# Kernel tuning notes

Measured on AMD Instinct MI355X. Metric: run time of the kernel, lower is better.

## Reference

```python
import jax, jax.numpy as jnp
import numpy as np

SCALE = 1.0 / 4.0      # alpha / dim
MULTIPLIER = 1.0

def _act(h):
    return jax.nn.gelu(h, approximate=False)  # torch nn.GELU(approximate='none')

def setup_inputs() -> dict:
    key = jax.random.key(0)
    ks = jax.random.split(key, 9)
    B, T, D = 64, 77, 768
    N, R = 1024, 4
    return {
        "x":     jax.random.normal(ks[0], (B, T, D), jnp.float32),
        "W_org": jax.random.normal(ks[1], (D, D), jnp.float32) * 0.02,
        "b_org": jax.random.normal(ks[2], (D,), jnp.float32) * 0.02,
        "w1":    jax.random.normal(ks[3], (N, D, R), jnp.float32) * 0.02,
        "b1":    jax.random.normal(ks[4], (N, R), jnp.float32) * 0.02,
        "mid_w": jax.random.normal(ks[5], (N, R, R), jnp.float32) * 0.02,
        "mid_b": jax.random.normal(ks[6], (N, R), jnp.float32) * 0.02,
        "w_out": jax.random.normal(ks[7], (N, R, D), jnp.float32) * 0.02,
        "b_out": jax.random.normal(ks[8], (N, D), jnp.float32) * 0.02,
    }

def reference(x, W_org, b_org, w1, b1, mid_w, mid_b, w_out, b_out):
    # per-concept low-rank MLP: h in [B, T, N, R]
    h = jnp.einsum('btd,ndh->btnh', x, w1) + b1[None, None]
    h = _act(h)
    # repeated 'h' in 'nhh' takes the diagonal of mid_w (elementwise scale),
    # exactly matching torch.einsum semantics in the source.
    h = jnp.einsum('btnh,nhh->btnh', h, mid_w) + mid_b[None, None]
    h = _act(h)
    # fuse out-projection with sum over concepts: sum_n (h_n @ w_out_n) + sum_n b_out_n
    up = jnp.einsum('btnh,nhd->btd', h, w_out) + jnp.sum(b_out, axis=0)
    org = x @ W_org.T + b_org
    return org + up * (MULTIPLIER * SCALE)
```

## Files before the change

kernel.cpp:

```cpp
#include <hip/hip_runtime.h>
#include <hip/hip_bf16.h>

#define M_TOK 4928
#define M_PAD 5120
#define M_GMM 4992
#define D_DIM 768
#define NR    4096

typedef __bf16 bf16;
typedef unsigned char u8;
typedef __attribute__((ext_vector_type(8))) __bf16 bf16x8;
typedef __attribute__((ext_vector_type(4))) float f32x4;
typedef __attribute__((address_space(1))) uint32_t gu32;
typedef __attribute__((address_space(3))) uint32_t su32;

#define GLDS(P, LDSP) \
  __builtin_amdgcn_global_load_lds((gu32*)(P), (su32*)(LDSP), 16, 0, 0)

__device__ __forceinline__ uint32_t pk_fp8x4(float a, float b, float c, float d) {
  uint32_t w = 0;
  w = (uint32_t)__builtin_amdgcn_cvt_pk_fp8_f32(a, b, (int)w, false);
  w = (uint32_t)__builtin_amdgcn_cvt_pk_fp8_f32(c, d, (int)w, true);
  return w;
}

__device__ __forceinline__ float act_fast(float v) {
  float e = __builtin_amdgcn_exp2f(v * -2.4554677f);
  return v * __builtin_amdgcn_rcpf(1.0f + e);
}

__device__ __forceinline__ int xcd_swizzle(int orig, int nwg) {
  const int q = nwg >> 3, r = nwg & 7;
  const int x = orig & 7, rest = orig >> 3;
  return (x < r ? x * (q + 1) : r * (q + 1) + (x - r) * q) + rest;
}


__global__ __launch_bounds__(256) void k_prep_x(const float* __restrict__ x,
                                                bf16* __restrict__ Xb) {
  int idx = (blockIdx.x * 256 + threadIdx.x) * 4;
  if (idx >= M_PAD * D_DIM) return;
  int m = idx / D_DIM;
  union { uint2 u; bf16 h[4]; } o;
  if (m < M_TOK) {
    float4 v = *(const float4*)(x + idx);
    o.h[0] = (bf16)v.x; o.h[1] = (bf16)v.y; o.h[2] = (bf16)v.z; o.h[3] = (bf16)v.w;
  } else {
    o.h[0] = o.h[1] = o.h[2] = o.h[3] = (bf16)0.0f;
  }
  *(uint2*)(Xb + idx) = o.u;
}

__global__ __launch_bounds__(256) void k_prep_xq(const float* __restrict__ x,
                                                 u8* __restrict__ Xq) {
  int idx = (blockIdx.x * 256 + threadIdx.x) * 4;
  if (idx >= M_PAD * D_DIM) return;
  int m = idx / D_DIM;
  uint32_t w = 0;
  if (m < M_TOK) {
    float4 v = *(const float4*)(x + idx);
    w = pk_fp8x4(v.x, v.y, v.z, v.w);
  }
  *(uint32_t*)(Xq + idx) = w;
}

__global__ __launch_bounds__(256) void k_prep_w1q(const float* __restrict__ w1,
                                                  u8* __restrict__ W1q) {
  int gid = blockIdx.x * 256 + threadIdx.x;
  int n = gid / 96, oct = gid % 96;
  const float4* src = (const float4*)w1 + (size_t)n * D_DIM + oct * 8;
  float e[4][8];
#pragma unroll
  for (int d = 0; d < 8; ++d) {
    float4 v = src[d];
    e[0][d] = v.x * 64.0f; e[1][d] = v.y * 64.0f;
    e[2][d] = v.z * 64.0f; e[3][d] = v.w * 64.0f;
  }
  size_t base = (size_t)n * 4 * D_DIM + oct * 8;
#pragma unroll
  for (int r = 0; r < 4; ++r) {
    uint2 o;
    o.x = pk_fp8x4(e[r][0], e[r][1], e[r][2], e[r][3]);
    o.y = pk_fp8x4(e[r][4], e[r][5], e[r][6], e[r][7]);
    *(uint2*)(W1q + base + (size_t)r * D_DIM) = o;
  }
}

__global__ __launch_bounds__(256) void k_prep_w2q(const float* __restrict__ w_out,
                                                  u8* __restrict__ W2q) {
  __shared__ float S[64 * 65];
  const int bk = blockIdx.x & 63, bd = blockIdx.x >> 6;
  const int k0 = bk * 64, d0 = bd * 64;
  const int tr = threadIdx.x >> 4;
  const int tc = (threadIdx.x & 15) * 4;
#pragma unroll
  for (int p = 0; p < 4; ++p) {
    const int kr = tr + p * 16;
    float4 v = *(const float4*)(w_out + (size_t)(k0 + kr) * D_DIM + d0 + tc);
    S[kr * 65 + tc + 0] = v.x; S[kr * 65 + tc + 1] = v.y;
    S[kr * 65 + tc + 2] = v.z; S[kr * 65 + tc + 3] = v.w;
  }
  __syncthreads();
#pragma unroll
  for (int p = 0; p < 4; ++p) {
    const int dr = tr + p * 16;
    uint32_t w = pk_fp8x4(16.0f * S[(tc + 0) * 65 + dr], 16.0f * S[(tc + 1) * 65 + dr],
                          16.0f * S[(tc + 2) * 65 + dr], 16.0f * S[(tc + 3) * 65 + dr]);
    *(uint32_t*)(W2q + (size_t)(d0 + dr) * NR + k0 + tc) = w;
  }
}

__global__ __launch_bounds__(256) void k_prep_worg(const float* __restrict__ W_org,
                                                   bf16* __restrict__ WorgB) {
  int idx = (blockIdx.x * 256 + threadIdx.x) * 4;
  if (idx >= D_DIM * D_DIM) return;
  float4 v = *(const float4*)(W_org + idx);
  union { uint2 u; bf16 h[4]; } o;
  o.h[0] = (bf16)v.x; o.h[1] = (bf16)v.y; o.h[2] = (bf16)v.z; o.h[3] = (bf16)v.w;
  *(uint2*)(WorgB + idx) = o.u;
}

__global__ __launch_bounds__(256) void k_bias_partial(const float* __restrict__ b_out,
                                                      float* __restrict__ partial) {
  int b = blockIdx.x;
  for (int d = threadIdx.x; d < D_DIM; d += 256) {
    float s = 0.0f;
    for (int n = b * 32; n < b * 32 + 32; ++n) s += b_out[n * D_DIM + d];
    partial[b * D_DIM + d] = s;
  }
}

__global__ __launch_bounds__(256) void k_bias_final2(const float* __restrict__ partial,
                                                     const float* __restrict__ b_org,
                                                     const float* __restrict__ mid_w,
                                                     float* __restrict__ bias_total,
                                                     float* __restrict__ diag) {
  int b = blockIdx.x;
  if (b < 3) {
    int d = b * 256 + threadIdx.x;
    if (d >= D_DIM) return;
    float s = 0.0f;
#pragma unroll
    for (int p = 0; p < 32; ++p) s += partial[p * D_DIM + d];
    bias_total[d] = b_org[d] + 0.25f * s;
  } else {
    int j = (b - 3) * 256 + threadIdx.x;
    diag[j] = mid_w[(j >> 2) * 16 + (j & 3) * 5];
  }
}


#define G1F_IT(S_, DO_STG, LAST_)                                               \
  {                                                                             \
    if (LAST_) { asm volatile("s_waitcnt vmcnt(0)" ::: "memory"); }             \
    else       { asm volatile("s_waitcnt vmcnt(4)" ::: "memory"); }             \
    asm volatile("s_barrier" ::: "memory");                                     \
    long a0[4], a1[4], b0[4], b1[4];                                            \
    _Pragma("unroll") for (int i = 0; i < 4; ++i) {                             \
      a0[i] = *(const long*)(&As[S_][aOff + i * 1024]);                         \
      a1[i] = *(const long*)(&As[S_][(aOff ^ 32) + i * 1024]);                  \
    }                                                                           \
    _Pragma("unroll") for (int j = 0; j < 4; ++j) {                             \
      b0[j] = *(const long*)(&Bs[S_][bOff + j * 1024]);                         \
      b1[j] = *(const long*)(&Bs[S_][(bOff ^ 32) + j * 1024]);                  \
    }                                                                           \
    if (DO_STG) {                                                               \
      GLDS(aP0, &As[((S_) + 2) % 3][ldsC0]);                                    \
      GLDS(aP1, &As[((S_) + 2) % 3][ldsC1]);                                    \
      GLDS(bP0, &Bs[((S_) + 2) % 3][ldsC0]);                                    \
      GLDS(bP1, &Bs[((S_) + 2) % 3][ldsC1]);                                    \
      aP0 += 64; aP1 += 64; bP0 += 64; bP1 += 64;                               \
    }                                                                           \
    _Pragma("unroll") for (int i = 0; i < 4; ++i)                               \
      _Pragma("unroll") for (int j = 0; j < 4; ++j)                             \
        acc[i][j] = __builtin_amdgcn_mfma_f32_16x16x32_fp8_fp8(b0[j], a0[i], acc[i][j], 0, 0, 0); \
    _Pragma("unroll") for (int i = 0; i < 4; ++i)                               \
      _Pragma("unroll") for (int j = 0; j < 4; ++j)                             \
        acc[i][j] = __builtin_amdgcn_mfma_f32_16x16x32_fp8_fp8(b1[j], a1[i], acc[i][j], 0, 0, 0); \
  }

__global__ __launch_bounds__(256) void k_gemm1(const u8* __restrict__ Xq,
                                               const u8* __restrict__ W1q,
                                               u8* __restrict__ H2q,
                                               const float* __restrict__ b1,
                                               const float* __restrict__ diag,
                                               const float* __restrict__ midb) {
  __shared__ u8 As[3][128 * 64];
  __shared__ u8 Bs[3][128 * 64];
  const int wgid = xcd_swizzle(blockIdx.x, 39 * 32);
  const int bmt = wgid >> 5;
  const int bnt = wgid & 31;
  const int m0 = bmt * 128, n0 = bnt * 128;
  const int lane = threadIdx.x & 63;
  const int wave = threadIdx.x >> 6;
  const int wm = wave >> 1, wn = wave & 1;
  const int lr = lane & 15, kg = lane >> 4;
  const int slotB = (((kg >> 1) ^ ((lr >> 1) & 3)) << 4) + ((kg & 1) << 3);
  const int aOff = (wm * 64 + lr) * 64 + slotB;
  const int bOff = (wn * 64 + lr) * 64 + slotB;

  const int src_slot = (lane & 3) ^ ((lane >> 3) & 3);
  const int srow = (wave * 2) * 16 + (lane >> 2);
  const u8* aP0 = Xq  + (size_t)(m0 + srow) * D_DIM + (src_slot << 4);
  const u8* aP1 = aP0 + 16 * D_DIM;
  const u8* bP0 = W1q + (size_t)(n0 + srow) * D_DIM + (src_slot << 4);
  const u8* bP1 = bP0 + 16 * D_DIM;
  const int ldsC0 = (wave * 2) * 1024, ldsC1 = ldsC0 + 1024;

  f32x4 acc[4][4];
#pragma unroll
  for (int i = 0; i < 4; ++i)
#pragma unroll
    for (int j = 0; j < 4; ++j) acc[i][j] = (f32x4)(0.0f);

  GLDS(aP0, &As[0][ldsC0]); GLDS(aP1, &As[0][ldsC1]);
  GLDS(bP0, &Bs[0][ldsC0]); GLDS(bP1, &Bs[0][ldsC1]);
  aP0 += 64; aP1 += 64; bP0 += 64; bP1 += 64;
  GLDS(aP0, &As[1][ldsC0]); GLDS(aP1, &As[1][ldsC1]);
  GLDS(bP0, &Bs[1][ldsC0]); GLDS(bP1, &Bs[1][ldsC1]);
  aP0 += 64; aP1 += 64; bP0 += 64; bP1 += 64;

  for (int g = 0; g < 3; ++g) {
    G1F_IT(0, true, false)
    G1F_IT(1, true, false)
    G1F_IT(2, true, false)
  }
  G1F_IT(0, true, false)
  G1F_IT(1, false, false)
  G1F_IT(2, false, true)

#pragma unroll
  for (int j = 0; j < 4; ++j) {
    const int jcb = n0 + wn * 64 + j * 16 + kg * 4;
    const float4 b1v = *(const float4*)(b1 + jcb);
    const float4 dgv = *(const float4*)(diag + jcb);
    const float4 mbv = *(const float4*)(midb + jcb);
#pragma unroll
    for (int i = 0; i < 4; ++i) {
      const int mr = m0 + wm * 64 + i * 16 + lr;
      float h, f0, f1, f2, f3;
      h = act_fast(fmaf(acc[i][j][0], 0.015625f, b1v.x)); f0 = act_fast(h * dgv.x + mbv.x);
      h = act_fast(fmaf(acc[i][j][1], 0.015625f, b1v.y)); f1 = act_fast(h * dgv.y + mbv.y);
      h = act_fast(fmaf(acc[i][j][2], 0.015625f, b1v.z)); f2 = act_fast(h * dgv.z + mbv.z);
      h = act_fast(fmaf(acc[i][j][3], 0.015625f, b1v.w)); f3 = act_fast(h * dgv.w + mbv.w);
      uint32_t w = pk_fp8x4(f0 * 128.0f, f1 * 128.0f, f2 * 128.0f, f3 * 128.0f);
      *(uint32_t*)(H2q + (size_t)mr * NR + jcb) = w;
    }
  }
}

__global__ __launch_bounds__(256) void k_gemm2a(const u8* __restrict__ H2q,
                                                const u8* __restrict__ W2q,
                                                bf16* __restrict__ padd) {
  __shared__ u8 As[3][128 * 64];
  __shared__ u8 Bs[3][128 * 64];
  const int wgid = xcd_swizzle(blockIdx.x, 39 * 6 * 4);
  const int bmt = wgid / 24;
  const int rem = wgid % 24;
  const int ks  = rem / 6;
  const int bnt = rem % 6;
  const int m0 = bmt * 128, n0 = bnt * 128;
  const int kbase = ks * 1024;
  const int lane = threadIdx.x & 63;
  const int wave = threadIdx.x >> 6;
  const int wm = wave >> 1, wn = wave & 1;
  const int lr = lane & 15, kg = lane >> 4;
  const int slotB = (((kg >> 1) ^ ((lr >> 1) & 3)) << 4) + ((kg & 1) << 3);
  const int aOff = (wm * 64 + lr) * 64 + slotB;
  const int bOff = (wn * 64 + lr) * 64 + slotB;

  const int src_slot = (lane & 3) ^ ((lane >> 3) & 3);
  const int srow = (wave * 2) * 16 + (lane >> 2);
  const u8* aP0 = H2q + (size_t)(m0 + srow) * NR + kbase + (src_slot << 4);
  const u8* aP1 = aP0 + 16 * NR;
  const u8* bP0 = W2q + (size_t)(n0 + srow) * NR + kbase + (src_slot << 4);
  const u8* bP1 = bP0 + 16 * NR;
  const int ldsC0 = (wave * 2) * 1024, ldsC1 = ldsC0 + 1024;

  f32x4 acc[4][4];
#pragma unroll
  for (int i = 0; i < 4; ++i)
#pragma unroll
    for (int j = 0; j < 4; ++j) acc[i][j] = (f32x4)(0.0f);

  GLDS(aP0, &As[0][ldsC0]); GLDS(aP1, &As[0][ldsC1]);
  GLDS(bP0, &Bs[0][ldsC0]); GLDS(bP1, &Bs[0][ldsC1]);
  aP0 += 64; aP1 += 64; bP0 += 64; bP1 += 64;
  GLDS(aP0, &As[1][ldsC0]); GLDS(aP1, &As[1][ldsC1]);
  GLDS(bP0, &Bs[1][ldsC0]); GLDS(bP1, &Bs[1][ldsC1]);
  aP0 += 64; aP1 += 64; bP0 += 64; bP1 += 64;

  for (int g = 0; g < 4; ++g) {
    G1F_IT(0, true, false)
    G1F_IT(1, true, false)
    G1F_IT(2, true, false)
  }
  G1F_IT(0, true, false)
  G1F_IT(1, true, false)
  G1F_IT(2, false, false)
  G1F_IT(0, false, true)

  bf16* dst = padd + (size_t)ks * M_TOK * D_DIM;
#pragma unroll
  for (int j = 0; j < 4; ++j) {
    const int cb = n0 + wn * 64 + j * 16 + kg * 4;
#pragma unroll
    for (int i = 0; i < 4; ++i) {
      const int mr = m0 + wm * 64 + i * 16 + lr;
      if (mr < M_TOK) {
        union { uint2 u; bf16 h[4]; } o;
        o.h[0] = (bf16)(acc[i][j][0] * 4.8828125e-4f);
        o.h[1] = (bf16)(acc[i][j][1] * 4.8828125e-4f);
        o.h[2] = (bf16)(acc[i][j][2] * 4.8828125e-4f);
        o.h[3] = (bf16)(acc[i][j][3] * 4.8828125e-4f);
        *(uint2*)(dst + (size_t)mr * D_DIM + cb) = o.u;
      }
    }
  }
}


#define G1B_IT(S_, DO_STG, LAST_)                                               \
  {                                                                             \
    if (LAST_) { asm volatile("s_waitcnt vmcnt(0)" ::: "memory"); }             \
    else       { asm volatile("s_waitcnt vmcnt(4)" ::: "memory"); }             \
    asm volatile("s_barrier" ::: "memory");                                     \
    bf16x8 a_[4], b_[4];                                                        \
    _Pragma("unroll") for (int i = 0; i < 4; ++i)                               \
      a_[i] = *(const bf16x8*)(&As[S_][aOff + i * 512]);                        \
    _Pragma("unroll") for (int j = 0; j < 4; ++j)                               \
      b_[j] = *(const bf16x8*)(&Bs[S_][bOff + j * 512]);                        \
    if (DO_STG) {                                                               \
      GLDS(aP0, &As[((S_) + 2) % 3][ldsC0]);                                    \
      GLDS(aP1, &As[((S_) + 2) % 3][ldsC1]);                                    \
      GLDS(bP0, &Bs[((S_) + 2) % 3][ldsC0]);                                    \
      GLDS(bP1, &Bs[((S_) + 2) % 3][ldsC1]);                                    \
      aP0 += 32; aP1 += 32; bP0 += 32; bP1 += 32;                               \
    }                                                                           \
    _Pragma("unroll") for (int i = 0; i < 4; ++i)                               \
      _Pragma("unroll") for (int j = 0; j < 4; ++j)                             \
        acc[i][j] = __builtin_amdgcn_mfma_f32_16x16x32_bf16(b_[j], a_[i], acc[i][j], 0, 0, 0); \
  }

__global__ __launch_bounds__(256) void k_gemm2b(const bf16* __restrict__ Xb,
                                                const bf16* __restrict__ WorgB,
                                                float* __restrict__ out,
                                                const float* __restrict__ bias) {
  __shared__ bf16 As[3][128 * 32];
  __shared__ bf16 Bs[3][128 * 32];
  const int wgid = xcd_swizzle(blockIdx.x, 39 * 6);
  const int bmt = wgid / 6;
  const int bnt = wgid % 6;
  const int m0 = bmt * 128, n0 = bnt * 128;
  const int lane = threadIdx.x & 63;
  const int wave = threadIdx.x >> 6;
  const int wm = wave >> 1, wn = wave & 1;
  const int lr = lane & 15, kg = lane >> 4;
  const int slot = (kg ^ ((lr >> 1) & 3)) << 3;
  const int aOff = (wm * 64 + lr) * 32 + slot;
  const int bOff = (wn * 64 + lr) * 32 + slot;

  const int src_slot = (lane & 3) ^ ((lane >> 3) & 3);
  const int srow = (wave * 2) * 16 + (lane >> 2);
  const bf16* aP0 = Xb    + (size_t)(m0 + srow) * D_DIM + (src_slot << 3);
  const bf16* aP1 = aP0 + 16 * D_DIM;
  const bf16* bP0 = WorgB + (size_t)(n0 + srow) * D_DIM + (src_slot << 3);
  const bf16* bP1 = bP0 + 16 * D_DIM;
  const int ldsC0 = (wave * 2) * 512, ldsC1 = ldsC0 + 512;

  f32x4 acc[4][4];
#pragma unroll
  for (int i = 0; i < 4; ++i)
#pragma unroll
    for (int j = 0; j < 4; ++j) acc[i][j] = (f32x4)(0.0f);

  GLDS(aP0, &As[0][ldsC0]); GLDS(aP1, &As[0][ldsC1]);
  GLDS(bP0, &Bs[0][ldsC0]); GLDS(bP1, &Bs[0][ldsC1]);
  aP0 += 32; aP1 += 32; bP0 += 32; bP1 += 32;
  GLDS(aP0, &As[1][ldsC0]); GLDS(aP1, &As[1][ldsC1]);
  GLDS(bP0, &Bs[1][ldsC0]); GLDS(bP1, &Bs[1][ldsC1]);
  aP0 += 32; aP1 += 32; bP0 += 32; bP1 += 32;

  for (int g = 0; g < 7; ++g) {
    G1B_IT(0, true, false)
    G1B_IT(1, true, false)
    G1B_IT(2, true, false)
  }
  G1B_IT(0, true, false)
  G1B_IT(1, false, false)
  G1B_IT(2, false, true)

#pragma unroll
  for (int j = 0; j < 4; ++j) {
    const int cb = n0 + wn * 64 + j * 16 + kg * 4;
    const f32x4 bv = *(const f32x4*)(bias + cb);
#pragma unroll
    for (int i = 0; i < 4; ++i) {
      const int mr = m0 + wm * 64 + i * 16 + lr;
      if (mr < M_TOK) {
        f32x4 o = acc[i][j] + bv;
        *(f32x4*)(out + (size_t)mr * D_DIM + cb) = o;
      }
    }
  }
}

__global__ __launch_bounds__(256) void k_reduce(const bf16* __restrict__ padd,
                                                float* __restrict__ out) {
  int idx = (blockIdx.x * 256 + threadIdx.x) * 4;
  if (idx >= M_TOK * D_DIM) return;
  float4 s = *(const float4*)(out + idx);
#pragma unroll
  for (int p = 0; p < 4; ++p) {
    union { uint2 u; bf16 h[4]; } v;
    v.u = *(const uint2*)(padd + (size_t)p * M_TOK * D_DIM + idx);
    s.x += (float)v.h[0]; s.y += (float)v.h[1];
    s.z += (float)v.h[2]; s.w += (float)v.h[3];
  }
  *(float4*)(out + idx) = s;
}


extern "C" void kernel_launch(void* const* d_in, const int* in_sizes, int n_in,
                              void* d_out, int out_size, void* d_ws, size_t ws_size,
                              hipStream_t stream) {
  const float* x     = (const float*)d_in[0];
  const float* W_org = (const float*)d_in[1];
  const float* b_org = (const float*)d_in[2];
  const float* w1    = (const float*)d_in[3];
  const float* b1    = (const float*)d_in[4];
  const float* mid_w = (const float*)d_in[5];
  const float* mid_b = (const float*)d_in[6];
  const float* w_out = (const float*)d_in[7];
  const float* b_out = (const float*)d_in[8];
  float* out = (float*)d_out;

  bf16* Xb    = (bf16*)d_ws;
  bf16* WorgB = Xb + (size_t)M_PAD * D_DIM;
  float* bias    = (float*)(WorgB + (size_t)D_DIM * D_DIM);
  float* partial = bias + 1024;
  float* diag    = partial + 32 * D_DIM;
  u8* Xq   = (u8*)(diag + NR);
  u8* W1q  = Xq  + (size_t)M_PAD * D_DIM;
  u8* W2q  = W1q + (size_t)NR * D_DIM;
  u8* H2q  = W2q + (size_t)D_DIM * NR;
  bf16* padd = (bf16*)(H2q + (size_t)M_GMM * NR);

  k_prep_x      <<<(M_PAD * D_DIM / 4) / 256, 256, 0, stream>>>(x, Xb);
  k_prep_xq     <<<(M_PAD * D_DIM / 4) / 256, 256, 0, stream>>>(x, Xq);
  k_prep_w1q    <<<384, 256, 0, stream>>>(w1, W1q);
  k_prep_w2q    <<<64 * 12, 256, 0, stream>>>(w_out, W2q);
  k_prep_worg   <<<(D_DIM * D_DIM / 4 + 255) / 256, 256, 0, stream>>>(W_org, WorgB);
  k_bias_partial<<<32, 256, 0, stream>>>(b_out, partial);
  k_bias_final2 <<<19, 256, 0, stream>>>(partial, b_org, mid_w, bias, diag);

  k_gemm1 <<<39 * 32, 256, 0, stream>>>(Xq, W1q, H2q, b1, diag, mid_b);
  k_gemm2a<<<39 * 6 * 4, 256, 0, stream>>>(H2q, W2q, padd);
  k_gemm2b<<<39 * 6, 256, 0, stream>>>(Xb, WorgB, out, bias);

  k_reduce<<<(M_TOK * D_DIM / 4) / 256, 256, 0, stream>>>(padd, out);
}
```

Baseline: 121.0 us.

## Interleave K dimension in fp8 operands to use 128-bit LDS reads in GEMMs

Permutes the K ordering of the fp8 operands (X, W1, W2 and the intermediate H2) so that each lane's two 8-byte MFMA fragments sit next to each other. Each lane can then fetch both k-halves with one 16-byte LDS read instead of two 8-byte reads. This halves the LDS read instruction count in the GEMM inner loops. The permutation must match across the prep kernels, the gemm1 epilogue store and gemm2, and any mismatch would corrupt the reduction.

```diff
diff --git a/kernel.cpp b/kernel.cpp
--- a/kernel.cpp
+++ b/kernel.cpp
@@ -11,11 +11,19 @@
 typedef unsigned char u8;
 typedef __attribute__((ext_vector_type(8))) __bf16 bf16x8;
 typedef __attribute__((ext_vector_type(4))) float f32x4;
+typedef __attribute__((ext_vector_type(2))) long longx2;
 typedef __attribute__((address_space(1))) uint32_t gu32;
 typedef __attribute__((address_space(3))) uint32_t su32;
 
 #define GLDS(P, LDSP) \
   __builtin_amdgcn_global_load_lds((gu32*)(P), (su32*)(LDSP), 16, 0, 0)
+
+__device__ __forceinline__ int ilv4(int k) {
+  return (k & ~63) + (k & 4) + (((k >> 5) & 1) << 3) + (((k >> 3) & 3) << 4);
+}
+__device__ __forceinline__ int ilv8(int k) {
+  return (k & ~63) + (((k >> 5) & 1) << 3) + (((k >> 3) & 3) << 4);
+}
 
 __device__ __forceinline__ uint32_t pk_fp8x4(float a, float b, float c, float d) {
   uint32_t w = 0;
@@ -55,13 +63,13 @@
                                                  u8* __restrict__ Xq) {
   int idx = (blockIdx.x * 256 + threadIdx.x) * 4;
   if (idx >= M_PAD * D_DIM) return;
-  int m = idx / D_DIM;
+  int m = idx / D_DIM, c = idx % D_DIM;
   uint32_t w = 0;
   if (m < M_TOK) {
     float4 v = *(const float4*)(x + idx);
     w = pk_fp8x4(v.x, v.y, v.z, v.w);
   }
-  *(uint32_t*)(Xq + idx) = w;
+  *(uint32_t*)(Xq + (size_t)m * D_DIM + ilv4(c)) = w;
 }
 
 __global__ __launch_bounds__(256) void k_prep_w1q(const float* __restrict__ w1,
@@ -76,13 +84,13 @@
     e[0][d] = v.x * 64.0f; e[1][d] = v.y * 64.0f;
     e[2][d] = v.z * 64.0f; e[3][d] = v.w * 64.0f;
   }
-  size_t base = (size_t)n * 4 * D_DIM + oct * 8;
+  const int cofs = ilv8(oct * 8);
 #pragma unroll
   for (int r = 0; r < 4; ++r) {
     uint2 o;
     o.x = pk_fp8x4(e[r][0], e[r][1], e[r][2], e[r][3]);
     o.y = pk_fp8x4(e[r][4], e[r][5], e[r][6], e[r][7]);
-    *(uint2*)(W1q + base + (size_t)r * D_DIM) = o;
+    *(uint2*)(W1q + (size_t)(n * 4 + r) * D_DIM + cofs) = o;
   }
 }
 
@@ -106,7 +114,7 @@
     const int dr = tr + p * 16;
     uint32_t w = pk_fp8x4(16.0f * S[(tc + 0) * 65 + dr], 16.0f * S[(tc + 1) * 65 + dr],
                           16.0f * S[(tc + 2) * 65 + dr], 16.0f * S[(tc + 3) * 65 + dr]);
-    *(uint32_t*)(W2q + (size_t)(d0 + dr) * NR + k0 + tc) = w;
+    *(uint32_t*)(W2q + (size_t)(d0 + dr) * NR + k0 + ilv4(tc)) = w;
   }
 }
 
@@ -155,15 +163,11 @@
     if (LAST_) { asm volatile("s_waitcnt vmcnt(0)" ::: "memory"); }             \
     else       { asm volatile("s_waitcnt vmcnt(4)" ::: "memory"); }             \
     asm volatile("s_barrier" ::: "memory");                                     \
-    long a0[4], a1[4], b0[4], b1[4];                                            \
-    _Pragma("unroll") for (int i = 0; i < 4; ++i) {                             \
-      a0[i] = *(const long*)(&As[S_][aOff + i * 1024]);                         \
-      a1[i] = *(const long*)(&As[S_][(aOff ^ 32) + i * 1024]);                  \
-    }                                                                           \
-    _Pragma("unroll") for (int j = 0; j < 4; ++j) {                             \
-      b0[j] = *(const long*)(&Bs[S_][bOff + j * 1024]);                         \
-      b1[j] = *(const long*)(&Bs[S_][(bOff ^ 32) + j * 1024]);                  \
-    }                                                                           \
+    longx2 av[4], bv[4];                                                        \
+    _Pragma("unroll") for (int i = 0; i < 4; ++i)                               \
+      av[i] = *(const longx2*)(&As[S_][aOff + i * 1024]);                       \
+    _Pragma("unroll") for (int j = 0; j < 4; ++j)                               \
+      bv[j] = *(const longx2*)(&Bs[S_][bOff + j * 1024]);                       \
     if (DO_STG) {                                                               \
       GLDS(aP0, &As[((S_) + 2) % 3][ldsC0]);                                    \
       GLDS(aP1, &As[((S_) + 2) % 3][ldsC1]);                                    \
@@ -173,10 +177,10 @@
     }                                                                           \
     _Pragma("unroll") for (int i = 0; i < 4; ++i)                               \
       _Pragma("unroll") for (int j = 0; j < 4; ++j)                             \
-        acc[i][j] = __builtin_amdgcn_mfma_f32_16x16x32_fp8_fp8(b0[j], a0[i], acc[i][j], 0, 0, 0); \
+        acc[i][j] = __builtin_amdgcn_mfma_f32_16x16x32_fp8_fp8(bv[j][0], av[i][0], acc[i][j], 0, 0, 0); \
     _Pragma("unroll") for (int i = 0; i < 4; ++i)                               \
       _Pragma("unroll") for (int j = 0; j < 4; ++j)                             \
-        acc[i][j] = __builtin_amdgcn_mfma_f32_16x16x32_fp8_fp8(b1[j], a1[i], acc[i][j], 0, 0, 0); \
+        acc[i][j] = __builtin_amdgcn_mfma_f32_16x16x32_fp8_fp8(bv[j][1], av[i][1], acc[i][j], 0, 0, 0); \
   }
 
 __global__ __launch_bounds__(256) void k_gemm1(const u8* __restrict__ Xq,
@@ -195,7 +199,7 @@
   const int wave = threadIdx.x >> 6;
   const int wm = wave >> 1, wn = wave & 1;
   const int lr = lane & 15, kg = lane >> 4;
-  const int slotB = (((kg >> 1) ^ ((lr >> 1) & 3)) << 4) + ((kg & 1) << 3);
+  const int slotB = (kg ^ ((lr >> 1) & 3)) << 4;
   const int aOff = (wm * 64 + lr) * 64 + slotB;
   const int bOff = (wn * 64 + lr) * 64 + slotB;
 
@@ -235,6 +239,8 @@
     const float4 b1v = *(const float4*)(b1 + jcb);
     const float4 dgv = *(const float4*)(diag + jcb);
     const float4 mbv = *(const float4*)(midb + jcb);
+    const int jq = j * 16 + kg * 4;
+    const int pl = (jq & 4) + (((jq >> 5) & 1) << 3) + (((jq >> 3) & 3) << 4);
 #pragma unroll
     for (int i = 0; i < 4; ++i) {
       const int mr = m0 + wm * 64 + i * 16 + lr;
@@ -244,7 +250,7 @@
       h = act_fast(fmaf(acc[i][j][2], 0.015625f, b1v.z)); f2 = act_fast(h * dgv.z + mbv.z);
       h = act_fast(fmaf(acc[i][j][3], 0.015625f, b1v.w)); f3 = act_fast(h * dgv.w + mbv.w);
       uint32_t w = pk_fp8x4(f0 * 128.0f, f1 * 128.0f, f2 * 128.0f, f3 * 128.0f);
-      *(uint32_t*)(H2q + (size_t)mr * NR + jcb) = w;
+      *(uint32_t*)(H2q + (size_t)mr * NR + (n0 + wn * 64) + pl) = w;
     }
   }
 }
@@ -265,7 +271,7 @@
   const int wave = threadIdx.x >> 6;
   const int wm = wave >> 1, wn = wave & 1;
   const int lr = lane & 15, kg = lane >> 4;
-  const int slotB = (((kg >> 1) ^ ((lr >> 1) & 3)) << 4) + ((kg & 1) << 3);
+  const int slotB = (kg ^ ((lr >> 1) & 3)) << 4;
   const int aOff = (wm * 64 + lr) * 64 + slotB;
   const int bOff = (wn * 64 + lr) * 64 + slotB;
 
```

New measurement: 118.7 us. Within noise of the previous version (-1.9%).
